# Optimization experiments

Hardware: AMD Instinct MI355X
Metric: run time of the kernel (lower is better)

Reference implementation:

```python
import jax, jax.numpy as jnp
import numpy as np

B, S1, S2 = 2, 2048, 2048
D1, D2 = 1024, 1024
H, K, V = 16, 64, 64


def setup_inputs() -> dict:
    key = jax.random.key(0)
    ks = jax.random.split(key, 8)
    x1 = jax.random.normal(ks[0], (B, S1, D1), dtype=jnp.float32)
    x2 = jax.random.normal(ks[1], (B, S2, D2), dtype=jnp.float32)
    weight_matrix = jax.random.uniform(ks[2], (B, H, S1, S2), dtype=jnp.float32)
    mask = jnp.ones((B, S1), dtype=jnp.int32)
    sc = 0.02
    Wq = jax.random.normal(ks[3], (H * K, D1), dtype=jnp.float32) * sc
    Wk = jax.random.normal(ks[4], (H * K, D2), dtype=jnp.float32) * sc
    Wv = jax.random.normal(ks[5], (H * V, D2), dtype=jnp.float32) * sc
    Wo = jax.random.normal(ks[6], (D1, H * V), dtype=jnp.float32) * sc
    bo = jnp.zeros((D1,), dtype=jnp.float32)
    return {"x1": x1, "x2": x2, "weight_matrix": weight_matrix, "mask": mask,
            "Wq": Wq, "Wk": Wk, "Wv": Wv, "Wo": Wo, "bo": bo}


def reference(x1, x2, weight_matrix, mask, Wq, Wk, Wv, Wo, bo):
    # 1x1 Conv1d == per-token linear; reshape weights to per-head form
    q = jnp.einsum('bsd,hkd->bhsk', x1, Wq.reshape(H, K, D1))   # [B,H,S1,K]
    k = jnp.einsum('bsd,hkd->bhsk', x2, Wk.reshape(H, K, D2))   # [B,H,S2,K]
    v = jnp.einsum('bsd,hvd->bhsv', x2, Wv.reshape(H, V, D2))   # [B,H,S2,V]

    attn = jnp.einsum('bhqk,bhsk->bhqs', q, k) / jnp.sqrt(jnp.float32(K))
    # mask is a query mask: [B,S1] -> broadcast over heads and keys
    attn = jnp.where(mask[:, None, :, None] == 0, -jnp.inf, attn)
    attn = attn * weight_matrix                                  # pre-softmax multiplicative bias
    attn = jax.nn.softmax(attn, axis=-1)
    # dropout p=0 (eval mode)

    out = jnp.einsum('bhqs,bhsv->bhqv', attn, v)                 # [B,H,S1,V]
    out = out.transpose(0, 1, 3, 2).reshape(B, H * V, S1)        # concat heads h-major
    return jnp.einsum('oc,bcq->bqo', Wo, out) + bo               # [B,S1,D1]
```

## Files before the change

kernel.cpp:

```cpp
#include <hip/hip_runtime.h>
#include <hip/hip_bf16.h>
#include <stdint.h>

typedef __attribute__((ext_vector_type(4))) float f32x4;
typedef __attribute__((ext_vector_type(8))) short bf16x8;
typedef __attribute__((ext_vector_type(8))) unsigned short u16x8;

__device__ __forceinline__ unsigned short f2bf(float f) {
  unsigned int u = __float_as_uint(f);
  u += 0x7fffu + ((u >> 16) & 1u);
  return (unsigned short)(u >> 16);
}

__device__ __forceinline__ unsigned int pk_bf16(float lo, float hi) {
  unsigned int r;
  asm("v_cvt_pk_bf16_f32 %0, %1, %2" : "=v"(r) : "v"(lo), "v"(hi));
  return r;
}

__device__ __forceinline__ void gld16(const void* g, void* l) {
  __builtin_amdgcn_global_load_lds(
      (const __attribute__((address_space(1))) unsigned int*)g,
      (__attribute__((address_space(3))) unsigned int*)l, 16, 0, 0);
}

__global__ __launch_bounds__(256) void cvt_kernel(const float* __restrict__ in,
                                                  unsigned short* __restrict__ out, int n4) {
  int stride = gridDim.x * blockDim.x;
  for (int i = blockIdx.x * blockDim.x + threadIdx.x; i < n4; i += stride) {
    float4 v = reinterpret_cast<const float4*>(in)[i];
    ushort4 o;
    o.x = f2bf(v.x); o.y = f2bf(v.y); o.z = f2bf(v.z); o.w = f2bf(v.w);
    reinterpret_cast<ushort4*>(out)[i] = o;
  }
}

template <int EPI>
__global__ __launch_bounds__(256) void gemm_bt(const unsigned short* __restrict__ A,
                                               const unsigned short* __restrict__ Bt,
                                               unsigned short* __restrict__ C,
                                               float* __restrict__ Cf,
                                               const float* __restrict__ bias,
                                               float scl, int M, int N, int Kd) {
  __shared__ unsigned short As[128 * 64];
  __shared__ unsigned short Bs[128 * 64];
  const int tid = threadIdx.x;
  const int lane = tid & 63;
  const int wid = tid >> 6;
  const int wm = wid >> 1, wn = wid & 1;
  const int lc = lane & 15, qr = lane >> 4;
  const int m0 = blockIdx.x * 128, n0 = blockIdx.y * 128;

  f32x4 acc[4][4];
#pragma unroll
  for (int i = 0; i < 4; i++)
#pragma unroll
    for (int j = 0; j < 4; j++) acc[i][j] = (f32x4)0.0f;

  for (int k0 = 0; k0 < Kd; k0 += 64) {
#pragma unroll
    for (int i = 0; i < 4; i++) {
      int c = i * 256 + tid;
      int row = c >> 3;
      int col = (c & 7) << 3;
      *reinterpret_cast<u16x8*>(&As[row * 64 + col]) =
          *reinterpret_cast<const u16x8*>(&A[(size_t)(m0 + row) * Kd + k0 + col]);
      *reinterpret_cast<u16x8*>(&Bs[row * 64 + col]) =
          *reinterpret_cast<const u16x8*>(&Bt[(size_t)(n0 + row) * Kd + k0 + col]);
    }
    __syncthreads();
#pragma unroll
    for (int kk = 0; kk < 2; kk++) {
      bf16x8 a[4], b[4];
#pragma unroll
      for (int mf = 0; mf < 4; mf++)
        a[mf] = *reinterpret_cast<const bf16x8*>(&As[(wm * 64 + mf * 16 + lc) * 64 + kk * 32 + qr * 8]);
#pragma unroll
      for (int nf = 0; nf < 4; nf++)
        b[nf] = *reinterpret_cast<const bf16x8*>(&Bs[(wn * 64 + nf * 16 + lc) * 64 + kk * 32 + qr * 8]);
#pragma unroll
      for (int mf = 0; mf < 4; mf++)
#pragma unroll
        for (int nf = 0; nf < 4; nf++)
          acc[mf][nf] = __builtin_amdgcn_mfma_f32_16x16x32_bf16(a[mf], b[nf], acc[mf][nf], 0, 0, 0);
    }
    __syncthreads();
  }

#pragma unroll
  for (int mf = 0; mf < 4; mf++) {
#pragma unroll
    for (int nf = 0; nf < 4; nf++) {
      const int row0 = m0 + wm * 64 + mf * 16 + qr * 4;
      const int col = n0 + wn * 64 + nf * 16 + lc;
#pragma unroll
      for (int r = 0; r < 4; r++) {
        float v = acc[mf][nf][r];
        int row = row0 + r;
        if (EPI == 0) {
          C[(size_t)row * N + col] = f2bf(v * scl);
        } else if (EPI == 1) {
          int bb = row >> 11, s2 = row & 2047;
          C[((size_t)(bb * 1024 + col)) * 2048 + s2] = f2bf(v);
        } else {
          Cf[(size_t)row * N + col] = v + bias[col];
        }
      }
    }
  }
}

__global__ __launch_bounds__(512, 4) void flash_kernel(const unsigned short* __restrict__ Qg,
                                                       const unsigned short* __restrict__ Kg,
                                                       const unsigned short* __restrict__ Vt,
                                                       const float* __restrict__ Wm,
                                                       const int* __restrict__ mask,
                                                       unsigned short* __restrict__ Og) {
  __shared__ __attribute__((aligned(16))) unsigned short K_lds[2][64][64];
  __shared__ __attribute__((aligned(16))) unsigned short V_lds[2][64][64];
  __shared__ unsigned short P_lds[8][16][72];
  const int tid = threadIdx.x;
  const int lane = tid & 63;
  const int wid = tid >> 6;
  const int lc = lane & 15, qr = lane >> 4;

  const int bx = blockIdx.x;
  const int nid = (bx & 7) * 64 + (bx >> 3);
  const int b = nid >> 8, h = (nid >> 4) & 15, qt = nid & 15;
  const int q0 = qt * 128 + wid * 16;

  bf16x8 aq[2];
#pragma unroll
  for (int kk = 0; kk < 2; kk++)
    aq[kk] = *reinterpret_cast<const bf16x8*>(
        &Qg[(size_t)(b * 2048 + q0 + lc) * 1024 + h * 64 + kk * 32 + qr * 8]);

  const float mbias = mask[b * 2048 + q0 + lc] ? 0.0f : -INFINITY;

  float m_run = -INFINITY, l_run = 0.0f;
  f32x4 o_acc[4];
#pragma unroll
  for (int vf = 0; vf < 4; vf++) o_acc[vf] = (f32x4)0.0f;

  const char* KbB = (const char*)Kg + (size_t)b * 2048 * 2048 + h * 128;
  const char* VbB = (const char*)Vt + ((size_t)b * 1024 + h * 64) * 4096;
  const float* wrow = Wm + ((size_t)((b * 16 + h) * 2048 + q0 + lc)) * 2048 + qr * 4;

  const int strow = tid >> 3;
  const int stcol = ((tid & 7) * 16) ^ ((strow & 7) << 4);
  const char* kst = KbB + (size_t)strow * 2048 + stcol;
  const char* vst = VbB + (size_t)strow * 4096 + stcol;
  char* kdst = (char*)K_lds + wid * 1024;
  char* vdst = (char*)V_lds + wid * 1024;
  const int rsw = (lc & 7) << 4;

  f32x4 wA[4], wB[4];

#define STAGEKV(TB, S0)                                                      \
  gld16(kst + (size_t)(S0) * 2048, kdst + (TB) * 8192);                      \
  gld16(vst + (size_t)(S0) * 2, vdst + (TB) * 8192);

#define LOADW(S0, W)                                                         \
  _Pragma("unroll") for (int f = 0; f < 4; f++)                              \
      W[f] = __builtin_nontemporal_load(                                     \
          reinterpret_cast<const f32x4*>(wrow + (S0) + f * 16));

#define TILE(T, BUF, WC, WN)                                                 \
  {                                                                          \
    if ((T) < 31) { STAGEKV((BUF) ^ 1, ((T) + 1) * 64); LOADW(((T) + 1) * 64, WN); } \
    const char* kb = (const char*)K_lds + (BUF) * 8192;                      \
    const char* vb = (const char*)V_lds + (BUF) * 8192;                      \
    f32x4 sacc[4];                                                           \
    _Pragma("unroll") for (int f = 0; f < 4; f++) sacc[f] = (f32x4)0.0f;     \
    _Pragma("unroll") for (int f = 0; f < 4; f++)                            \
    _Pragma("unroll") for (int kk = 0; kk < 2; kk++) {                       \
      bf16x8 kf = *reinterpret_cast<const bf16x8*>(                          \
          kb + (f * 16 + lc) * 128 + ((kk * 64 + qr * 16) ^ rsw));           \
      sacc[f] = __builtin_amdgcn_mfma_f32_16x16x32_bf16(kf, aq[kk], sacc[f], 0, 0, 0); \
    }                                                                        \
    float tm = -INFINITY;                                                    \
    _Pragma("unroll") for (int f = 0; f < 4; f++)                            \
    _Pragma("unroll") for (int r = 0; r < 4; r++) {                          \
      float v = fmaf(sacc[f][r], WC[f][r], mbias);                           \
      sacc[f][r] = v;                                                        \
      tm = fmaxf(tm, v);                                                     \
    }                                                                        \
    tm = fmaxf(tm, __shfl_xor(tm, 16));                                      \
    tm = fmaxf(tm, __shfl_xor(tm, 32));                                      \
    const float mn = fmaxf(m_run, tm);                                       \
    const float sc = __expf(m_run - mn);                                     \
    m_run = mn;                                                              \
    float rs = 0.0f;                                                         \
    _Pragma("unroll") for (int f = 0; f < 4; f++)                            \
    _Pragma("unroll") for (int r = 0; r < 4; r++) {                          \
      float p = __expf(sacc[f][r] - mn);                                     \
      sacc[f][r] = p;                                                        \
      rs += p;                                                               \
    }                                                                        \
    rs += __shfl_xor(rs, 16);                                                \
    rs += __shfl_xor(rs, 32);                                                \
    l_run = l_run * sc + rs;                                                 \
    _Pragma("unroll") for (int vf = 0; vf < 4; vf++)                         \
    _Pragma("unroll") for (int r = 0; r < 4; r++) o_acc[vf][r] *= sc;        \
    _Pragma("unroll") for (int f = 0; f < 4; f++) {                          \
      unsigned int u0 = pk_bf16(sacc[f][0], sacc[f][1]);                     \
      unsigned int u1 = pk_bf16(sacc[f][2], sacc[f][3]);                     \
      const int kbse = f * 16 + qr * 4;                                      \
      *reinterpret_cast<unsigned int*>(&P_lds[wid][lc][kbse]) = u0;          \
      *reinterpret_cast<unsigned int*>(&P_lds[wid][lc][kbse + 2]) = u1;      \
    }                                                                        \
    _Pragma("unroll") for (int kk = 0; kk < 2; kk++) {                       \
      bf16x8 pb = *reinterpret_cast<const bf16x8*>(                          \
          &P_lds[wid][lc][kk * 32 + qr * 8]);                                \
      _Pragma("unroll") for (int vf = 0; vf < 4; vf++) {                     \
        bf16x8 vr = *reinterpret_cast<const bf16x8*>(                        \
            vb + (vf * 16 + lc) * 128 + ((kk * 64 + qr * 16) ^ rsw));        \
        o_acc[vf] = __builtin_amdgcn_mfma_f32_16x16x32_bf16(vr, pb, o_acc[vf], 0, 0, 0); \
      }                                                                      \
    }                                                                        \
    __syncthreads();                                                         \
  }

  STAGEKV(0, 0);
  LOADW(0, wA);
  __syncthreads();
#pragma unroll 1
  for (int t = 0; t < 32; t += 2) {
    TILE(t, 0, wA, wB);
    TILE(t + 1, 1, wB, wA);
  }

  const float inv = 1.0f / l_run;
#pragma unroll
  for (int vf = 0; vf < 4; vf++)
#pragma unroll
    for (int r = 0; r < 4; r++)
      Og[(size_t)(b * 2048 + q0 + lc) * 1024 + h * 64 + vf * 16 + qr * 4 + r] =
          f2bf(o_acc[vf][r] * inv);
}

extern "C" void kernel_launch(void* const* d_in, const int* in_sizes, int n_in,
                              void* d_out, int out_size, void* d_ws, size_t ws_size,
                              hipStream_t stream) {
  (void)in_sizes; (void)n_in; (void)out_size; (void)ws_size;
  const float* x1 = (const float*)d_in[0];
  const float* x2 = (const float*)d_in[1];
  const float* Wm = (const float*)d_in[2];
  const int* mask = (const int*)d_in[3];
  const float* Wq = (const float*)d_in[4];
  const float* Wk = (const float*)d_in[5];
  const float* Wv = (const float*)d_in[6];
  const float* Wo = (const float*)d_in[7];
  const float* bo = (const float*)d_in[8];

  char* ws = (char*)d_ws;
  const size_t SZ_X = (size_t)4096 * 1024 * 2;
  const size_t SZ_W = (size_t)1024 * 1024 * 2;
  unsigned short* x1b = (unsigned short*)(ws + 0);
  unsigned short* x2b = (unsigned short*)(ws + SZ_X);
  unsigned short* Wqb = (unsigned short*)(ws + 2 * SZ_X);
  unsigned short* Wkb = (unsigned short*)(ws + 2 * SZ_X + SZ_W);
  unsigned short* Wvb = (unsigned short*)(ws + 2 * SZ_X + 2 * SZ_W);
  unsigned short* Wob = (unsigned short*)(ws + 2 * SZ_X + 3 * SZ_W);
  unsigned short* Qb  = (unsigned short*)(ws + 2 * SZ_X + 4 * SZ_W);
  unsigned short* Kb  = (unsigned short*)(ws + 3 * SZ_X + 4 * SZ_W);
  unsigned short* Vtb = (unsigned short*)(ws + 4 * SZ_X + 4 * SZ_W);
  unsigned short* Ob  = (unsigned short*)(ws + 5 * SZ_X + 4 * SZ_W);

  cvt_kernel<<<2048, 256, 0, stream>>>(x1, x1b, 4096 * 1024 / 4);
  cvt_kernel<<<2048, 256, 0, stream>>>(x2, x2b, 4096 * 1024 / 4);
  cvt_kernel<<<512, 256, 0, stream>>>(Wq, Wqb, 1024 * 1024 / 4);
  cvt_kernel<<<512, 256, 0, stream>>>(Wk, Wkb, 1024 * 1024 / 4);
  cvt_kernel<<<512, 256, 0, stream>>>(Wv, Wvb, 1024 * 1024 / 4);
  cvt_kernel<<<512, 256, 0, stream>>>(Wo, Wob, 1024 * 1024 / 4);

  dim3 gg(32, 8);
  gemm_bt<0><<<gg, 256, 0, stream>>>(x1b, Wqb, Qb, nullptr, nullptr, 0.125f, 4096, 1024, 1024);
  gemm_bt<0><<<gg, 256, 0, stream>>>(x2b, Wkb, Kb, nullptr, nullptr, 1.0f, 4096, 1024, 1024);
  gemm_bt<1><<<gg, 256, 0, stream>>>(x2b, Wvb, Vtb, nullptr, nullptr, 1.0f, 4096, 1024, 1024);

  flash_kernel<<<512, 512, 0, stream>>>(Qb, Kb, Vtb, Wm, mask, Ob);

  gemm_bt<2><<<gg, 256, 0, stream>>>(Ob, Wob, nullptr, (float*)d_out, bo, 1.0f, 4096, 1024, 1024);
}
```

Measured before the change: 272.1 us.

## Triple-buffer K/V staging with two-tile lookahead and fine-grained vmcnt waits

Moves the flash attention main loop from double to triple buffering of K/V tiles in LDS and of the weight-matrix register fragments, so each tile prefetches two tiles ahead. The full __syncthreads is replaced by an explicit s_waitcnt vmcnt(N) plus s_barrier, which waits only for the older loads, and sched_barriers pin the order in which loads are issued. The aim is to hide more global-load latency, mainly the large streamed weight_matrix reads. In exchange it uses more LDS and registers, which may hurt occupancy under launch_bounds(512,4), and the hand-counted vmcnt values must match the actual number of outstanding loads to stay correct.

Result: slower. 324.0 us (+19.1%).

```diff
diff --git a/kernel.cpp b/kernel.cpp
--- a/kernel.cpp
+++ b/kernel.cpp
@@ -23,6 +23,10 @@
       (const __attribute__((address_space(1))) unsigned int*)g,
       (__attribute__((address_space(3))) unsigned int*)l, 16, 0, 0);
 }
+
+#define VMCNT_(N) asm volatile("s_waitcnt vmcnt(" #N ") lgkmcnt(0)" ::: "memory")
+#define VMCNT(N) VMCNT_(N)
+#define SB0 __builtin_amdgcn_sched_barrier(0)
 
 __global__ __launch_bounds__(256) void cvt_kernel(const float* __restrict__ in,
                                                   unsigned short* __restrict__ out, int n4) {
@@ -116,8 +120,8 @@
                                                        const float* __restrict__ Wm,
                                                        const int* __restrict__ mask,
                                                        unsigned short* __restrict__ Og) {
-  __shared__ __attribute__((aligned(16))) unsigned short K_lds[2][64][64];
-  __shared__ __attribute__((aligned(16))) unsigned short V_lds[2][64][64];
+  __shared__ __attribute__((aligned(16))) unsigned short K_lds[3][64][64];
+  __shared__ __attribute__((aligned(16))) unsigned short V_lds[3][64][64];
   __shared__ unsigned short P_lds[8][16][72];
   const int tid = threadIdx.x;
   const int lane = tid & 63;
@@ -154,7 +158,7 @@
   char* vdst = (char*)V_lds + wid * 1024;
   const int rsw = (lc & 7) << 4;
 
-  f32x4 wA[4], wB[4];
+  f32x4 wA[4], wB[4], wC[4];
 
 #define STAGEKV(TB, S0)                                                      \
   gld16(kst + (size_t)(S0) * 2048, kdst + (TB) * 8192);                      \
@@ -165,9 +169,14 @@
       W[f] = __builtin_nontemporal_load(                                     \
           reinterpret_cast<const f32x4*>(wrow + (S0) + f * 16));
 
-#define TILE(T, BUF, WC, WN)                                                 \
+#define TILE(T, BUF, BUF2, WC, WN, WAITN, DOBAR)                             \
   {                                                                          \
-    if ((T) < 31) { STAGEKV((BUF) ^ 1, ((T) + 1) * 64); LOADW(((T) + 1) * 64, WN); } \
+    if ((T) + 2 < 32) {                                                      \
+      STAGEKV(BUF2, ((T) + 2) * 64);                                         \
+      SB0;                                                                   \
+      LOADW(((T) + 2) * 64, WN);                                             \
+      SB0;                                                                   \
+    }                                                                        \
     const char* kb = (const char*)K_lds + (BUF) * 8192;                      \
     const char* vb = (const char*)V_lds + (BUF) * 8192;                      \
     f32x4 sacc[4];                                                           \
@@ -218,17 +227,28 @@
         o_acc[vf] = __builtin_amdgcn_mfma_f32_16x16x32_bf16(vr, pb, o_acc[vf], 0, 0, 0); \
       }                                                                      \
     }                                                                        \
-    __syncthreads();                                                         \
+    if (DOBAR) { VMCNT(WAITN); __builtin_amdgcn_s_barrier(); }               \
   }
 
   STAGEKV(0, 0);
+  SB0;
   LOADW(0, wA);
-  __syncthreads();
+  SB0;
+  STAGEKV(1, 64);
+  SB0;
+  LOADW(64, wB);
+  SB0;
+  VMCNT(10);
+  __builtin_amdgcn_s_barrier();
+
 #pragma unroll 1
-  for (int t = 0; t < 32; t += 2) {
-    TILE(t, 0, wA, wB);
-    TILE(t + 1, 1, wB, wA);
-  }
+  for (int t = 0; t < 30; t += 3) {
+    TILE(t,     0, 2, wA, wC, 10, 1);
+    TILE(t + 1, 1, 0, wB, wA, 10, 1);
+    TILE(t + 2, 2, 1, wC, wB, 10, 1);
+  }
+  TILE(30, 0, 2, wA, wC, 4, 1);
+  TILE(31, 1, 0, wB, wA, 0, 0);
 
   const float inv = 1.0f / l_run;
 #pragma unroll
```

## Split keys across waves per 16-query block and merge softmax partials in LDS

Applied to the files above, without the earlier changes.

The flash kernel now gives each block 16 queries, with the 8 waves splitting the key dimension (split-K style) instead of splitting queries. K and V are read straight from global into registers, and only the fp32 weight_matrix tile is staged through LDS with async loads. The per-wave softmax states are then combined through shared memory at the end. The aim is 8x more blocks and a coalesced stream of the large weight_matrix, at the cost of re-reading K and V for every 16-query block and an extra cross-wave reduction.

New measurement: 407.0 us. 49.6% more time.

```diff
diff --git a/kernel.cpp b/kernel.cpp
--- a/kernel.cpp
+++ b/kernel.cpp
@@ -116,18 +116,18 @@
                                                        const float* __restrict__ Wm,
                                                        const int* __restrict__ mask,
                                                        unsigned short* __restrict__ Og) {
-  __shared__ __attribute__((aligned(16))) unsigned short K_lds[2][64][64];
-  __shared__ __attribute__((aligned(16))) unsigned short V_lds[2][64][64];
-  __shared__ unsigned short P_lds[8][16][72];
+  __shared__ __attribute__((aligned(16))) float W_smem[2][16][256];
+  __shared__ __attribute__((aligned(16))) unsigned short P_smem[8][16][40];
+  __shared__ __attribute__((aligned(16))) float mlbuf[2][8][16];
   const int tid = threadIdx.x;
   const int lane = tid & 63;
   const int wid = tid >> 6;
   const int lc = lane & 15, qr = lane >> 4;
 
   const int bx = blockIdx.x;
-  const int nid = (bx & 7) * 64 + (bx >> 3);
-  const int b = nid >> 8, h = (nid >> 4) & 15, qt = nid & 15;
-  const int q0 = qt * 128 + wid * 16;
+  const int nid = (bx & 7) * 512 + (bx >> 3);
+  const int b = nid >> 11, h = (nid >> 7) & 15, qt = nid & 127;
+  const int q0 = qt * 16;
 
   bf16x8 aq[2];
 #pragma unroll
@@ -142,101 +142,129 @@
 #pragma unroll
   for (int vf = 0; vf < 4; vf++) o_acc[vf] = (f32x4)0.0f;
 
-  const char* KbB = (const char*)Kg + (size_t)b * 2048 * 2048 + h * 128;
-  const char* VbB = (const char*)Vt + ((size_t)b * 1024 + h * 64) * 4096;
-  const float* wrow = Wm + ((size_t)((b * 16 + h) * 2048 + q0 + lc)) * 2048 + qr * 4;
-
-  const int strow = tid >> 3;
-  const int stcol = ((tid & 7) * 16) ^ ((strow & 7) << 4);
-  const char* kst = KbB + (size_t)strow * 2048 + stcol;
-  const char* vst = VbB + (size_t)strow * 4096 + stcol;
-  char* kdst = (char*)K_lds + wid * 1024;
-  char* vdst = (char*)V_lds + wid * 1024;
+  const unsigned short* Kb = Kg + (size_t)(b * 2048) * 1024 + h * 64;
+  const unsigned short* Vb = Vt + (size_t)(b * 1024 + h * 64) * 2048;
+
+  const char* wb0 = (const char*)Wm +
+      ((size_t)((b * 16 + h) * 2048 + q0 + wid * 2 + 0)) * 8192 +
+      ((lane * 16) ^ (((wid * 2 + 0) & 7) << 4));
+  const char* wb1 = (const char*)Wm +
+      ((size_t)((b * 16 + h) * 2048 + q0 + wid * 2 + 1)) * 8192 +
+      ((lane * 16) ^ (((wid * 2 + 1) & 7) << 4));
   const int rsw = (lc & 7) << 4;
 
-  f32x4 wA[4], wB[4];
-
-#define STAGEKV(TB, S0)                                                      \
-  gld16(kst + (size_t)(S0) * 2048, kdst + (TB) * 8192);                      \
-  gld16(vst + (size_t)(S0) * 2, vdst + (TB) * 8192);
-
-#define LOADW(S0, W)                                                         \
-  _Pragma("unroll") for (int f = 0; f < 4; f++)                              \
-      W[f] = __builtin_nontemporal_load(                                     \
-          reinterpret_cast<const f32x4*>(wrow + (S0) + f * 16));
-
-#define TILE(T, BUF, WC, WN)                                                 \
-  {                                                                          \
-    if ((T) < 31) { STAGEKV((BUF) ^ 1, ((T) + 1) * 64); LOADW(((T) + 1) * 64, WN); } \
-    const char* kb = (const char*)K_lds + (BUF) * 8192;                      \
-    const char* vb = (const char*)V_lds + (BUF) * 8192;                      \
-    f32x4 sacc[4];                                                           \
-    _Pragma("unroll") for (int f = 0; f < 4; f++) sacc[f] = (f32x4)0.0f;     \
-    _Pragma("unroll") for (int f = 0; f < 4; f++)                            \
-    _Pragma("unroll") for (int kk = 0; kk < 2; kk++) {                       \
-      bf16x8 kf = *reinterpret_cast<const bf16x8*>(                          \
-          kb + (f * 16 + lc) * 128 + ((kk * 64 + qr * 16) ^ rsw));           \
-      sacc[f] = __builtin_amdgcn_mfma_f32_16x16x32_bf16(kf, aq[kk], sacc[f], 0, 0, 0); \
-    }                                                                        \
-    float tm = -INFINITY;                                                    \
-    _Pragma("unroll") for (int f = 0; f < 4; f++)                            \
-    _Pragma("unroll") for (int r = 0; r < 4; r++) {                          \
-      float v = fmaf(sacc[f][r], WC[f][r], mbias);                           \
-      sacc[f][r] = v;                                                        \
-      tm = fmaxf(tm, v);                                                     \
-    }                                                                        \
-    tm = fmaxf(tm, __shfl_xor(tm, 16));                                      \
-    tm = fmaxf(tm, __shfl_xor(tm, 32));                                      \
-    const float mn = fmaxf(m_run, tm);                                       \
-    const float sc = __expf(m_run - mn);                                     \
-    m_run = mn;                                                              \
-    float rs = 0.0f;                                                         \
-    _Pragma("unroll") for (int f = 0; f < 4; f++)                            \
-    _Pragma("unroll") for (int r = 0; r < 4; r++) {                          \
-      float p = __expf(sacc[f][r] - mn);                                     \
-      sacc[f][r] = p;                                                        \
-      rs += p;                                                               \
-    }                                                                        \
-    rs += __shfl_xor(rs, 16);                                                \
-    rs += __shfl_xor(rs, 32);                                                \
-    l_run = l_run * sc + rs;                                                 \
-    _Pragma("unroll") for (int vf = 0; vf < 4; vf++)                         \
-    _Pragma("unroll") for (int r = 0; r < 4; r++) o_acc[vf][r] *= sc;        \
-    _Pragma("unroll") for (int f = 0; f < 4; f++) {                          \
-      unsigned int u0 = pk_bf16(sacc[f][0], sacc[f][1]);                     \
-      unsigned int u1 = pk_bf16(sacc[f][2], sacc[f][3]);                     \
-      const int kbse = f * 16 + qr * 4;                                      \
-      *reinterpret_cast<unsigned int*>(&P_lds[wid][lc][kbse]) = u0;          \
-      *reinterpret_cast<unsigned int*>(&P_lds[wid][lc][kbse + 2]) = u1;      \
-    }                                                                        \
-    _Pragma("unroll") for (int kk = 0; kk < 2; kk++) {                       \
-      bf16x8 pb = *reinterpret_cast<const bf16x8*>(                          \
-          &P_lds[wid][lc][kk * 32 + qr * 8]);                                \
-      _Pragma("unroll") for (int vf = 0; vf < 4; vf++) {                     \
-        bf16x8 vr = *reinterpret_cast<const bf16x8*>(                        \
-            vb + (vf * 16 + lc) * 128 + ((kk * 64 + qr * 16) ^ rsw));        \
-        o_acc[vf] = __builtin_amdgcn_mfma_f32_16x16x32_bf16(vr, pb, o_acc[vf], 0, 0, 0); \
-      }                                                                      \
-    }                                                                        \
-    __syncthreads();                                                         \
-  }
-
-  STAGEKV(0, 0);
-  LOADW(0, wA);
+#define STW(BUF, ST)                                                         \
+  gld16(wb0 + (size_t)(ST) * 1024, &W_smem[BUF][wid * 2][0]);                \
+  gld16(wb1 + (size_t)(ST) * 1024, &W_smem[BUF][wid * 2 + 1][0]);
+
+  STW(0, 0);
   __syncthreads();
+
 #pragma unroll 1
-  for (int t = 0; t < 32; t += 2) {
-    TILE(t, 0, wA, wB);
-    TILE(t + 1, 1, wB, wA);
-  }
-
-  const float inv = 1.0f / l_run;
-#pragma unroll
-  for (int vf = 0; vf < 4; vf++)
-#pragma unroll
-    for (int r = 0; r < 4; r++)
-      Og[(size_t)(b * 2048 + q0 + lc) * 1024 + h * 64 + vf * 16 + qr * 4 + r] =
-          f2bf(o_acc[vf][r] * inv);
+  for (int st = 0; st < 8; ++st) {
+    const int buf = st & 1;
+    const int kb0 = st * 256 + wid * 32;
+
+    bf16x8 kf0 = *reinterpret_cast<const bf16x8*>(&Kb[(size_t)(kb0 + lc) * 1024 + qr * 8]);
+    bf16x8 kf1 = *reinterpret_cast<const bf16x8*>(&Kb[(size_t)(kb0 + lc) * 1024 + 32 + qr * 8]);
+    bf16x8 kf2 = *reinterpret_cast<const bf16x8*>(&Kb[(size_t)(kb0 + 16 + lc) * 1024 + qr * 8]);
+    bf16x8 kf3 = *reinterpret_cast<const bf16x8*>(&Kb[(size_t)(kb0 + 16 + lc) * 1024 + 32 + qr * 8]);
+    bf16x8 vr0 = *reinterpret_cast<const bf16x8*>(&Vb[(size_t)(0 * 16 + lc) * 2048 + kb0 + qr * 8]);
+    bf16x8 vr1 = *reinterpret_cast<const bf16x8*>(&Vb[(size_t)(1 * 16 + lc) * 2048 + kb0 + qr * 8]);
+    bf16x8 vr2 = *reinterpret_cast<const bf16x8*>(&Vb[(size_t)(2 * 16 + lc) * 2048 + kb0 + qr * 8]);
+    bf16x8 vr3 = *reinterpret_cast<const bf16x8*>(&Vb[(size_t)(3 * 16 + lc) * 2048 + kb0 + qr * 8]);
+    __builtin_amdgcn_sched_barrier(0);
+    if (st < 7) { STW(buf ^ 1, st + 1); }
+    __builtin_amdgcn_sched_barrier(0);
+
+    const char* wrl = (const char*)&W_smem[buf][0][0] + lc * 1024;
+    f32x4 w0 = *reinterpret_cast<const f32x4*>(wrl + ((wid * 128 + qr * 16) ^ rsw));
+    f32x4 w1 = *reinterpret_cast<const f32x4*>(wrl + ((wid * 128 + 64 + qr * 16) ^ rsw));
+
+    f32x4 sacc0 = (f32x4)0.0f, sacc1 = (f32x4)0.0f;
+    sacc0 = __builtin_amdgcn_mfma_f32_16x16x32_bf16(kf0, aq[0], sacc0, 0, 0, 0);
+    sacc0 = __builtin_amdgcn_mfma_f32_16x16x32_bf16(kf1, aq[1], sacc0, 0, 0, 0);
+    sacc1 = __builtin_amdgcn_mfma_f32_16x16x32_bf16(kf2, aq[0], sacc1, 0, 0, 0);
+    sacc1 = __builtin_amdgcn_mfma_f32_16x16x32_bf16(kf3, aq[1], sacc1, 0, 0, 0);
+
+    float p0 = fmaf(sacc0[0], w0[0], mbias), p1 = fmaf(sacc0[1], w0[1], mbias);
+    float p2 = fmaf(sacc0[2], w0[2], mbias), p3 = fmaf(sacc0[3], w0[3], mbias);
+    float p4 = fmaf(sacc1[0], w1[0], mbias), p5 = fmaf(sacc1[1], w1[1], mbias);
+    float p6 = fmaf(sacc1[2], w1[2], mbias), p7 = fmaf(sacc1[3], w1[3], mbias);
+
+    float tm = fmaxf(fmaxf(fmaxf(p0, p1), fmaxf(p2, p3)),
+                     fmaxf(fmaxf(p4, p5), fmaxf(p6, p7)));
+    tm = fmaxf(tm, __shfl_xor(tm, 16));
+    tm = fmaxf(tm, __shfl_xor(tm, 32));
+    const float mn = fmaxf(m_run, tm);
+    const float sc = __expf(m_run - mn);
+    m_run = mn;
+    p0 = __expf(p0 - mn); p1 = __expf(p1 - mn);
+    p2 = __expf(p2 - mn); p3 = __expf(p3 - mn);
+    p4 = __expf(p4 - mn); p5 = __expf(p5 - mn);
+    p6 = __expf(p6 - mn); p7 = __expf(p7 - mn);
+    float rs = ((p0 + p1) + (p2 + p3)) + ((p4 + p5) + (p6 + p7));
+    rs += __shfl_xor(rs, 16);
+    rs += __shfl_xor(rs, 32);
+    l_run = l_run * sc + rs;
+#pragma unroll
+    for (int vf = 0; vf < 4; vf++)
+#pragma unroll
+      for (int r = 0; r < 4; r++) o_acc[vf][r] *= sc;
+
+    unsigned int u0 = pk_bf16(p0, p1), u1 = pk_bf16(p2, p3);
+    unsigned int u2 = pk_bf16(p4, p5), u3 = pk_bf16(p6, p7);
+    *reinterpret_cast<unsigned int*>(&P_smem[wid][lc][qr * 4]) = u0;
+    *reinterpret_cast<unsigned int*>(&P_smem[wid][lc][qr * 4 + 2]) = u1;
+    *reinterpret_cast<unsigned int*>(&P_smem[wid][lc][16 + qr * 4]) = u2;
+    *reinterpret_cast<unsigned int*>(&P_smem[wid][lc][16 + qr * 4 + 2]) = u3;
+
+    bf16x8 pb = *reinterpret_cast<const bf16x8*>(&P_smem[wid][lc][qr * 8]);
+    o_acc[0] = __builtin_amdgcn_mfma_f32_16x16x32_bf16(vr0, pb, o_acc[0], 0, 0, 0);
+    o_acc[1] = __builtin_amdgcn_mfma_f32_16x16x32_bf16(vr1, pb, o_acc[1], 0, 0, 0);
+    o_acc[2] = __builtin_amdgcn_mfma_f32_16x16x32_bf16(vr2, pb, o_acc[2], 0, 0, 0);
+    o_acc[3] = __builtin_amdgcn_mfma_f32_16x16x32_bf16(vr3, pb, o_acc[3], 0, 0, 0);
+
+    __syncthreads();
+  }
+
+  if (lane < 16) {
+    mlbuf[0][wid][lane] = m_run;
+    mlbuf[1][wid][lane] = l_run;
+  }
+  __syncthreads();
+
+  float mstar = mlbuf[0][0][lc];
+#pragma unroll
+  for (int w = 1; w < 8; w++) mstar = fmaxf(mstar, mlbuf[0][w][lc]);
+  const float fac = __expf(m_run - mstar);
+  float* obuf = (float*)W_smem;
+#pragma unroll
+  for (int vf = 0; vf < 4; vf++) {
+    f32x4 t = o_acc[vf];
+    t[0] *= fac; t[1] *= fac; t[2] *= fac; t[3] *= fac;
+    *reinterpret_cast<f32x4*>(&obuf[((wid * 16 + lc) << 6) + vf * 16 + qr * 4]) = t;
+  }
+  __syncthreads();
+
+  {
+    const int o = tid * 2, q = o >> 6, v = o & 63;
+    float mq = mlbuf[0][0][q];
+#pragma unroll
+    for (int w = 1; w < 8; w++) mq = fmaxf(mq, mlbuf[0][w][q]);
+    float lq = 0.0f, s0 = 0.0f, s1 = 0.0f;
+#pragma unroll
+    for (int w = 0; w < 8; w++) {
+      lq += __expf(mlbuf[0][w][q] - mq) * mlbuf[1][w][q];
+      s0 += obuf[((w * 16 + q) << 6) + v];
+      s1 += obuf[((w * 16 + q) << 6) + v + 1];
+    }
+    const float inv = 1.0f / lq;
+    ushort2 st2;
+    st2.x = f2bf(s0 * inv);
+    st2.y = f2bf(s1 * inv);
+    *reinterpret_cast<ushort2*>(&Og[(size_t)(b * 2048 + q0 + q) * 1024 + h * 64 + v]) = st2;
+  }
 }
 
 extern "C" void kernel_launch(void* const* d_in, const int* in_sizes, int n_in,
@@ -279,7 +307,7 @@
   gemm_bt<0><<<gg, 256, 0, stream>>>(x2b, Wkb, Kb, nullptr, nullptr, 1.0f, 4096, 1024, 1024);
   gemm_bt<1><<<gg, 256, 0, stream>>>(x2b, Wvb, Vtb, nullptr, nullptr, 1.0f, 4096, 1024, 1024);
 
-  flash_kernel<<<512, 512, 0, stream>>>(Qb, Kb, Vtb, Wm, mask, Ob);
+  flash_kernel<<<4096, 512, 0, stream>>>(Qb, Kb, Vtb, Wm, mask, Ob);
 
   gemm_bt<2><<<gg, 256, 0, stream>>>(Ob, Wob, nullptr, (float*)d_out, bo, 1.0f, 4096, 1024, 1024);
 }
```
